# Performance work log

Hardware: AMD Instinct MI355X
Metric: run time of the kernel (lower is better)

The kernel has to match this reference:

```python
import jax, jax.numpy as jnp
import numpy as np

B, S, D = 2, 2048, 2048
H, KVH, DH = 32, 8, 64
G = H // KVH  # num_key_value_groups
SCALE = DH ** -0.5
NEG = -1e9


def rotate_half(x):
    x1, x2 = jnp.split(x, 2, axis=-1)
    return jnp.concatenate([-x2, x1], axis=-1)


def setup_inputs() -> dict:
    key = jax.random.key(0)
    ks = jax.random.split(key, 6)
    hidden_states = jax.random.normal(ks[0], (B, S, D), dtype=jnp.float32)
    # RoPE tables (base 10000), shape [B, S, DH]
    inv_freq = 1.0 / (10000.0 ** (np.arange(0, DH, 2, dtype=np.float32) / DH))
    t = np.arange(S, dtype=np.float32)
    freqs = np.outer(t, inv_freq)                     # [S, DH/2]
    emb = np.concatenate([freqs, freqs], axis=-1)     # [S, DH]
    cos = jnp.broadcast_to(jnp.cos(emb)[None], (B, S, DH)).astype(jnp.float32)
    sin = jnp.broadcast_to(jnp.sin(emb)[None], (B, S, DH)).astype(jnp.float32)
    # additive causal mask [B, 1, S, S]
    causal = np.tril(np.ones((S, S), dtype=bool))
    mask = jnp.asarray(np.where(causal, 0.0, NEG).astype(np.float32))
    attention_mask = jnp.broadcast_to(mask[None, None], (B, 1, S, S))
    std = 0.02
    Wq = jax.random.normal(ks[1], (H * DH, D), dtype=jnp.float32) * std
    Wk = jax.random.normal(ks[2], (KVH * DH, D), dtype=jnp.float32) * std
    Wv = jax.random.normal(ks[3], (KVH * DH, D), dtype=jnp.float32) * std
    Wo = jax.random.normal(ks[4], (D, H * DH), dtype=jnp.float32) * std
    return {"hidden_states": hidden_states, "cos": cos, "sin": sin,
            "attention_mask": attention_mask, "Wq": Wq, "Wk": Wk, "Wv": Wv, "Wo": Wo}


def reference(hidden_states, cos, sin, attention_mask, Wq, Wk, Wv, Wo):
    b, s, d = hidden_states.shape
    # projections -> [B, heads, S, DH]
    q = (hidden_states @ Wq.T).reshape(b, s, H, DH).transpose(0, 2, 1, 3)
    k = (hidden_states @ Wk.T).reshape(b, s, KVH, DH).transpose(0, 2, 1, 3)
    v = (hidden_states @ Wv.T).reshape(b, s, KVH, DH).transpose(0, 2, 1, 3)
    # RoPE (unsqueeze_dim=1)
    c = cos[:, None]  # [B,1,S,DH]
    sn = sin[:, None]
    q = q * c + rotate_half(q) * sn
    k = k * c + rotate_half(k) * sn
    # GQA: repeat kv heads
    k = jnp.repeat(k, G, axis=1)
    v = jnp.repeat(v, G, axis=1)
    scores = jnp.einsum("bhqd,bhkd->bhqk", q, k) * SCALE + attention_mask
    attn = jax.nn.softmax(scores.astype(jnp.float32), axis=-1).astype(q.dtype)
    out = jnp.einsum("bhqk,bhkd->bhqd", attn, v)          # [B,H,S,DH]
    out = out.transpose(0, 2, 1, 3).reshape(b, s, H * DH)  # [B,S,H*DH]
    return out @ Wo.T
```

## Files before the change

kernel.cpp:

```cpp
#include <hip/hip_runtime.h>

typedef unsigned short u16;
typedef __attribute__((ext_vector_type(8))) short s16x8;
typedef __attribute__((ext_vector_type(4))) float f32x4;
typedef __attribute__((ext_vector_type(4))) unsigned short u16x4;

#define MFMA16(a, b, c) __builtin_amdgcn_mfma_f32_16x16x32_bf16(a, b, c, 0, 0, 0)

__device__ __forceinline__ u16 f2bf(float f) {
  unsigned u = __builtin_bit_cast(unsigned, f);
  u += 0x7fffu + ((u >> 16) & 1u);
  return (u16)(u >> 16);
}

__device__ __forceinline__ u16 f2bf_fast(float f) {
  return (u16)((__builtin_bit_cast(unsigned, f) + 0x8000u) >> 16);
}

__device__ __forceinline__ void async16(const void* g, void* l) {
  __builtin_amdgcn_global_load_lds(
      (const __attribute__((address_space(1))) void*)g,
      (__attribute__((address_space(3))) void*)l, 16, 0, 0);
}

__device__ __forceinline__ s16x8 ld8(const u16* p) { return *(const s16x8*)p; }

#define PRE 0.18033688011112042f

__global__ __launch_bounds__(256) void cvt_all(
    const float* __restrict__ X, const float* __restrict__ Wq,
    const float* __restrict__ Wk, const float* __restrict__ Wv,
    const float* __restrict__ Wo, u16* __restrict__ out) {
  long e = (long)(blockIdx.x * 256 + threadIdx.x) * 4;
  const float* src;
  if (e < 8388608L) src = X + e;
  else if (e < 12582912L) src = Wq + (e - 8388608L);
  else if (e < 13631488L) src = Wk + (e - 12582912L);
  else if (e < 14680064L) src = Wv + (e - 13631488L);
  else src = Wo + (e - 14680064L);
  float4 v = *(const float4*)src;
  u16x4 o = {f2bf(v.x), f2bf(v.y), f2bf(v.z), f2bf(v.w)};
  *(u16x4*)(out + e) = o;
}

enum { EPI_QKV = 0, EPI_OUT = 1 };

template <int EPI>
__global__ __launch_bounds__(256) void gemm_nt(
    const u16* __restrict__ A, const u16* __restrict__ Bm,
    const float* __restrict__ cosp, const float* __restrict__ sinp,
    u16* __restrict__ Qo, u16* __restrict__ Ko, u16* __restrict__ Vo,
    float* __restrict__ Co, int K) {
  __shared__ u16 SM[16384];
  const int t = threadIdx.x;
  const int lane = t & 63;
  const int w = t >> 6, wm = w >> 1, wn = w & 1;
  const int quad = lane >> 4, c16 = lane & 15;
  const int m0 = blockIdx.y * 128, n0 = blockIdx.x * 128;

  f32x4 acc[4][4];
  const f32x4 zero = {0.f, 0.f, 0.f, 0.f};
#pragma unroll
  for (int i = 0; i < 4; ++i)
#pragma unroll
    for (int j = 0; j < 4; ++j) acc[i][j] = zero;

  const u16* gA[2];
  const u16* gB[2];
  int lof[2];
#pragma unroll
  for (int p = 0; p < 2; ++p) {
    int c = t + p * 256;
    int dr = c >> 3, k8 = (c & 7) ^ (dr & 7);
    int row = 2 * dr + (k8 >> 2), col = (k8 & 3) * 8;
    gA[p] = A + (size_t)(m0 + row) * K + col;
    gB[p] = Bm + (size_t)(n0 + row) * K + col;
    lof[p] = c * 8;
  }

  int aoff[4], boff[4];
#pragma unroll
  for (int i = 0; i < 4; ++i) {
    int rowA = wm * 64 + i * 16 + c16;
    int drA = rowA >> 1;
    int chA = (((rowA & 1) << 2) | quad) ^ (drA & 7);
    aoff[i] = drA * 64 + chA * 8;
    int rowB = wn * 64 + i * 16 + c16;
    int drB = rowB >> 1;
    int chB = (((rowB & 1) << 2) | quad) ^ (drB & 7);
    boff[i] = 4096 + drB * 64 + chB * 8;
  }

#pragma unroll
  for (int p = 0; p < 2; ++p) {
    async16(gA[p], &SM[lof[p]]);
    async16(gB[p], &SM[4096 + lof[p]]);
  }

  const int niter = K >> 5;
  for (int kt = 0; kt < niter; ++kt) {
    const int cb = (kt & 1) * 8192;
    __syncthreads();
    if (kt + 1 < niter) {
      const int nb = 8192 - cb;
#pragma unroll
      for (int p = 0; p < 2; ++p) {
        gA[p] += 32;
        gB[p] += 32;
        async16(gA[p], &SM[nb + lof[p]]);
        async16(gB[p], &SM[nb + 4096 + lof[p]]);
      }
    }
    s16x8 af[4], bfr[4];
#pragma unroll
    for (int i = 0; i < 4; ++i) af[i] = ld8(&SM[cb + aoff[i]]);
#pragma unroll
    for (int j = 0; j < 4; ++j) bfr[j] = ld8(&SM[cb + boff[j]]);
#pragma unroll
    for (int i = 0; i < 4; ++i)
#pragma unroll
      for (int j = 0; j < 4; ++j) acc[i][j] = MFMA16(af[i], bfr[j], acc[i][j]);
  }

  if (EPI == EPI_OUT) {
#pragma unroll
    for (int i = 0; i < 4; ++i)
#pragma unroll
      for (int r = 0; r < 4; ++r) {
        int m = m0 + wm * 64 + i * 16 + quad * 4 + r;
        float* dst = Co + (size_t)m * 2048 + n0 + wn * 64 + c16;
#pragma unroll
        for (int j = 0; j < 4; ++j) dst[j * 16] = acc[i][j][r];
      }
  } else if (n0 >= 2560) {
    __syncthreads();
#pragma unroll
    for (int i = 0; i < 4; ++i)
#pragma unroll
      for (int r = 0; r < 4; ++r) {
        int sl = wm * 64 + i * 16 + quad * 4 + r;
#pragma unroll
        for (int j = 0; j < 4; ++j) {
          int dl = wn * 64 + j * 16 + c16;
          SM[dl * 128 + (((sl >> 3) ^ (dl & 15)) * 8) + (sl & 7)] =
              f2bf(acc[i][j][r]);
        }
      }
    __syncthreads();
    int bb = m0 >> 11, m0s = m0 & 2047;
#pragma unroll
    for (int p = 0; p < 8; ++p) {
      int q = p * 256 + t;
      int dl = q >> 4, k = q & 15;
      s16x8 vrow = ld8(&SM[dl * 128 + ((k ^ (dl & 15)) * 8)]);
      int nab = n0 + dl;
      int kvh = (nab - 2560) >> 6, dh = nab & 63;
      *(s16x8*)(Vo + ((size_t)(bb * 8 + kvh) * 64 + dh) * 2048 + m0s + k * 8) =
          vrow;
    }
  } else {
    const int nbase = n0 + wn * 64;
#pragma unroll
    for (int i = 0; i < 4; ++i)
#pragma unroll
      for (int r = 0; r < 4; ++r) {
        int m = m0 + wm * 64 + i * 16 + quad * 4 + r;
        int b = m >> 11, s = m & 2047;
        if (nbase < 2048) {
          int h = nbase >> 6;
          size_t base = ((size_t)(b * 32 + h) * 2048 + s) * 64;
#pragma unroll
          for (int j = 0; j < 2; ++j) {
            int d = j * 16 + c16;
            float v1 = acc[i][j][r], v2 = acc[i][j + 2][r];
            float c1 = cosp[m * 64 + d], s1 = sinp[m * 64 + d];
            float c2 = cosp[m * 64 + d + 32], s2 = sinp[m * 64 + d + 32];
            Qo[base + d] = f2bf((v1 * c1 - v2 * s1) * PRE);
            Qo[base + d + 32] = f2bf((v2 * c2 + v1 * s2) * PRE);
          }
        } else {
          int h = (nbase - 2048) >> 6;
          size_t base = ((size_t)(b * 8 + h) * 2048 + s) * 64;
#pragma unroll
          for (int j = 0; j < 2; ++j) {
            int d = j * 16 + c16;
            float v1 = acc[i][j][r], v2 = acc[i][j + 2][r];
            float c1 = cosp[m * 64 + d], s1 = sinp[m * 64 + d];
            float c2 = cosp[m * 64 + d + 32], s2 = sinp[m * 64 + d + 32];
            Ko[base + d] = f2bf(v1 * c1 - v2 * s1);
            Ko[base + d + 32] = f2bf(v2 * c2 + v1 * s2);
          }
        }
      }
  }
}

__global__ __launch_bounds__(256) void attn(const u16* __restrict__ Q,
                                            const u16* __restrict__ Kg,
                                            const u16* __restrict__ Vg,
                                            u16* __restrict__ O) {
  __shared__ u16 Ks[2][4096];
  __shared__ u16 Vs[2][4096];
  __shared__ u16 Ps[8192];
  const int t = threadIdx.x;
  const int lane = t & 63;
  const int w = t >> 6;
  const int quad = lane >> 4, c16 = lane & 15;
  const int bh = blockIdx.y;
  const int b = bh >> 5, h = bh & 31;
  const int kvh = h >> 2;

  const u16* Qbase = Q + ((size_t)(b * 32 + h) * 2048) * 64;
  const u16* Kbase = Kg + ((size_t)(b * 8 + kvh) * 2048) * 64;
  const u16* Vbase = Vg + ((size_t)(b * 8 + kvh) * 64) * 2048;

  const int sr0 = t >> 3, sc0 = ((t & 7) ^ (sr0 & 7)) * 8;
  const int sr1 = (t + 256) >> 3, sc1 = (((t + 256) & 7) ^ (sr1 & 7)) * 8;

  for (int ph = 0; ph < 2; ++ph) {
    const int qt = ph ? 15 - blockIdx.x : blockIdx.x;
    const int q0 = qt * 128;

    s16x8 qa[2][2];
#pragma unroll
    for (int im = 0; im < 2; ++im)
#pragma unroll
      for (int c = 0; c < 2; ++c)
        qa[im][c] = ld8(Qbase + (size_t)(q0 + w * 32 + im * 16 + c16) * 64 +
                        c * 32 + quad * 8);

    f32x4 oacc[2][4];
    const f32x4 zero = {0.f, 0.f, 0.f, 0.f};
    float lacc[2][4];
#pragma unroll
    for (int im = 0; im < 2; ++im)
#pragma unroll
      for (int r = 0; r < 4; ++r) lacc[im][r] = 0.f;
#pragma unroll
    for (int im = 0; im < 2; ++im)
#pragma unroll
      for (int dt = 0; dt < 4; ++dt) oacc[im][dt] = zero;

    const int nkt = 2 * qt + 2;

    __syncthreads();
    {
      const u16* kg = Kbase;
      async16(kg + sr0 * 64 + sc0, &Ks[0][t * 8]);
      async16(kg + sr1 * 64 + sc1, &Ks[0][t * 8 + 2048]);
      async16(Vbase + (size_t)sr0 * 2048 + sc0, &Vs[0][t * 8]);
      async16(Vbase + (size_t)sr1 * 2048 + sc1, &Vs[0][t * 8 + 2048]);
    }

    for (int kt = 0; kt < nkt; ++kt) {
      const int cur = kt & 1;
      __syncthreads();
      if (kt + 1 < nkt) {
        const int nxt = 1 - cur;
        const u16* kg = Kbase + (kt + 1) * 4096;
        async16(kg + sr0 * 64 + sc0, &Ks[nxt][t * 8]);
        async16(kg + sr1 * 64 + sc1, &Ks[nxt][t * 8 + 2048]);
        async16(Vbase + (size_t)sr0 * 2048 + (kt + 1) * 64 + sc0,
                &Vs[nxt][t * 8]);
        async16(Vbase + (size_t)sr1 * 2048 + (kt + 1) * 64 + sc1,
                &Vs[nxt][t * 8 + 2048]);
      }
      const u16* Kb = Ks[cur];
      const u16* Vb = Vs[cur];

#pragma unroll
      for (int im = 0; im < 2; ++im) {
        f32x4 sc[4];
#pragma unroll
        for (int in = 0; in < 4; ++in) sc[in] = zero;
#pragma unroll
        for (int c = 0; c < 2; ++c)
#pragma unroll
          for (int in = 0; in < 4; ++in) {
            s16x8 kf = ld8(&Kb[(in * 16 + c16) * 64 +
                               (((c * 4 + quad) ^ (c16 & 7)) * 8)]);
            sc[in] = MFMA16(qa[im][c], kf, sc[in]);
          }
        const int rbase = q0 + w * 32 + im * 16;
        if (kt * 64 + 63 > rbase) {
#pragma unroll
          for (int in = 0; in < 4; ++in) {
            int kcol = kt * 64 + in * 16 + c16;
#pragma unroll
            for (int r = 0; r < 4; ++r)
              if (kcol > rbase + quad * 4 + r) sc[in][r] = -1e30f;
          }
        }
#pragma unroll
        for (int in = 0; in < 4; ++in)
#pragma unroll
          for (int r = 0; r < 4; ++r) {
            float p = exp2f(sc[in][r]);
            lacc[im][r] += p;
            int row = im * 16 + quad * 4 + r;
            Ps[w * 2048 + row * 64 +
               (((in * 2 + (c16 >> 3)) ^ (row & 7)) * 8) + (c16 & 7)] =
                f2bf_fast(p);
          }
      }

#pragma unroll
      for (int c = 0; c < 2; ++c) {
        const int swz = ((c * 4 + quad) ^ (c16 & 7)) * 8;
        s16x8 pf[2];
#pragma unroll
        for (int im = 0; im < 2; ++im)
          pf[im] = ld8(&Ps[w * 2048 + (im * 16 + c16) * 64 + swz]);
#pragma unroll
        for (int dt = 0; dt < 4; ++dt) {
          s16x8 vf = ld8(&Vb[(dt * 16 + c16) * 64 + swz]);
#pragma unroll
          for (int im = 0; im < 2; ++im)
            oacc[im][dt] = MFMA16(pf[im], vf, oacc[im][dt]);
        }
      }
    }

#pragma unroll
    for (int im = 0; im < 2; ++im) {
      float inv[4];
#pragma unroll
      for (int r = 0; r < 4; ++r) {
        float v = lacc[im][r];
        v += __shfl_xor(v, 1);
        v += __shfl_xor(v, 2);
        v += __shfl_xor(v, 4);
        v += __shfl_xor(v, 8);
        inv[r] = 1.f / v;
      }
#pragma unroll
      for (int dt = 0; dt < 4; ++dt)
#pragma unroll
        for (int r = 0; r < 4; ++r) {
          int s = q0 + w * 32 + im * 16 + quad * 4 + r;
          O[((size_t)(b * 2048 + s)) * 2048 + h * 64 + dt * 16 + c16] =
              f2bf(oacc[im][dt][r] * inv[r]);
        }
    }
  }
}

extern "C" void kernel_launch(void* const* d_in, const int* in_sizes, int n_in,
                              void* d_out, int out_size, void* d_ws,
                              size_t ws_size, hipStream_t stream) {
  const float* X = (const float*)d_in[0];
  const float* cosp = (const float*)d_in[1];
  const float* sinp = (const float*)d_in[2];
  const float* Wq = (const float*)d_in[4];
  const float* Wk = (const float*)d_in[5];
  const float* Wv = (const float*)d_in[6];
  const float* Wo = (const float*)d_in[7];
  float* out = (float*)d_out;

  u16* Xb = (u16*)d_ws;
  u16* Wqkv = Xb + 8388608;
  u16* Wob = Wqkv + 6291456;
  u16* Qr = Wob + 4194304;
  u16* Kr = Qr + 8388608;
  u16* Vt = Kr + 2097152;
  u16* Ob = Vt + 2097152;

  cvt_all<<<18432, 256, 0, stream>>>(X, Wq, Wk, Wv, Wo, Xb);

  gemm_nt<EPI_QKV><<<dim3(24, 32), 256, 0, stream>>>(
      Xb, Wqkv, cosp, sinp, Qr, Kr, Vt, nullptr, 2048);

  attn<<<dim3(8, 64), 256, 0, stream>>>(Qr, Kr, Vt, Ob);

  gemm_nt<EPI_OUT><<<dim3(16, 32), 256, 0, stream>>>(
      Ob, Wob, nullptr, nullptr, nullptr, nullptr, nullptr, out, 2048);
}
```

Before: 328.5 us.

## Rewrite attention inner loop with 32x32 MFMA and register-resident P via permlane swap

The attention kernel switches from 16x16x32 to 32x32x16 bf16 MFMAs and computes S transposed (K times Q), so each lane holds scores for a single query row. Probabilities are packed to bf16 with v_cvt_pk_bf16_f32 and rearranged across half-waves with permlane32_swap to form the PV operand directly in registers, removing the P round trip through shared memory. Fully masked 32-key sub-blocks are skipped and the row-sum reduction becomes one shuffle plus a small LDS broadcast. The risks are higher register pressure from the 16-wide accumulators and a fragile lane and register mapping.

```diff
diff --git a/kernel.cpp b/kernel.cpp
--- a/kernel.cpp
+++ b/kernel.cpp
@@ -3,9 +3,12 @@
 typedef unsigned short u16;
 typedef __attribute__((ext_vector_type(8))) short s16x8;
 typedef __attribute__((ext_vector_type(4))) float f32x4;
+typedef __attribute__((ext_vector_type(16))) float f32x16;
 typedef __attribute__((ext_vector_type(4))) unsigned short u16x4;
+typedef __attribute__((ext_vector_type(4))) unsigned int u32x4;
 
 #define MFMA16(a, b, c) __builtin_amdgcn_mfma_f32_16x16x32_bf16(a, b, c, 0, 0, 0)
+#define MFMA32(a, b, c) __builtin_amdgcn_mfma_f32_32x32x16_bf16(a, b, c, 0, 0, 0)
 
 __device__ __forceinline__ u16 f2bf(float f) {
   unsigned u = __builtin_bit_cast(unsigned, f);
@@ -13,10 +16,6 @@
   return (u16)(u >> 16);
 }
 
-__device__ __forceinline__ u16 f2bf_fast(float f) {
-  return (u16)((__builtin_bit_cast(unsigned, f) + 0x8000u) >> 16);
-}
-
 __device__ __forceinline__ void async16(const void* g, void* l) {
   __builtin_amdgcn_global_load_lds(
       (const __attribute__((address_space(1))) void*)g,
@@ -24,6 +23,12 @@
 }
 
 __device__ __forceinline__ s16x8 ld8(const u16* p) { return *(const s16x8*)p; }
+
+__device__ __forceinline__ unsigned cvtpk(float lo, float hi) {
+  unsigned r;
+  asm("v_cvt_pk_bf16_f32 %0, %1, %2" : "=v"(r) : "v"(lo), "v"(hi));
+  return r;
+}
 
 #define PRE 0.18033688011112042f
 
@@ -201,11 +206,11 @@
                                             u16* __restrict__ O) {
   __shared__ u16 Ks[2][4096];
   __shared__ u16 Vs[2][4096];
-  __shared__ u16 Ps[8192];
+  __shared__ float Lred[128];
   const int t = threadIdx.x;
   const int lane = t & 63;
   const int w = t >> 6;
-  const int quad = lane >> 4, c16 = lane & 15;
+  const int l31 = lane & 31, hi = lane >> 5;
   const int bh = blockIdx.y;
   const int b = bh >> 5, h = bh & 31;
   const int kvh = h >> 2;
@@ -217,37 +222,35 @@
   const int sr0 = t >> 3, sc0 = ((t & 7) ^ (sr0 & 7)) * 8;
   const int sr1 = (t + 256) >> 3, sc1 = (((t + 256) & 7) ^ (sr1 & 7)) * 8;
 
+  int off8[4];
+#pragma unroll
+  for (int c = 0; c < 4; ++c) off8[c] = ((2 * c + hi) ^ (l31 & 7)) * 8;
+  const int rbB = l31 * 64;
+
   for (int ph = 0; ph < 2; ++ph) {
     const int qt = ph ? 15 - blockIdx.x : blockIdx.x;
     const int q0 = qt * 128;
-
-    s16x8 qa[2][2];
-#pragma unroll
-    for (int im = 0; im < 2; ++im)
-#pragma unroll
-      for (int c = 0; c < 2; ++c)
-        qa[im][c] = ld8(Qbase + (size_t)(q0 + w * 32 + im * 16 + c16) * 64 +
-                        c * 32 + quad * 8);
-
-    f32x4 oacc[2][4];
-    const f32x4 zero = {0.f, 0.f, 0.f, 0.f};
-    float lacc[2][4];
-#pragma unroll
-    for (int im = 0; im < 2; ++im)
-#pragma unroll
-      for (int r = 0; r < 4; ++r) lacc[im][r] = 0.f;
-#pragma unroll
-    for (int im = 0; im < 2; ++im)
-#pragma unroll
-      for (int dt = 0; dt < 4; ++dt) oacc[im][dt] = zero;
+    const int rbase = q0 + w * 32;
+    const int qrow = rbase + l31;
+
+    s16x8 qf[4];
+#pragma unroll
+    for (int dc = 0; dc < 4; ++dc)
+      qf[dc] = ld8(Qbase + (size_t)qrow * 64 + dc * 16 + hi * 8);
+
+    f32x16 oacc[2];
+#pragma unroll
+    for (int dn = 0; dn < 2; ++dn)
+#pragma unroll
+      for (int r = 0; r < 16; ++r) oacc[dn][r] = 0.f;
+    float lacc = 0.f;
 
     const int nkt = 2 * qt + 2;
 
     __syncthreads();
     {
-      const u16* kg = Kbase;
-      async16(kg + sr0 * 64 + sc0, &Ks[0][t * 8]);
-      async16(kg + sr1 * 64 + sc1, &Ks[0][t * 8 + 2048]);
+      async16(Kbase + sr0 * 64 + sc0, &Ks[0][t * 8]);
+      async16(Kbase + sr1 * 64 + sc1, &Ks[0][t * 8 + 2048]);
       async16(Vbase + (size_t)sr0 * 2048 + sc0, &Vs[0][t * 8]);
       async16(Vbase + (size_t)sr1 * 2048 + sc1, &Vs[0][t * 8 + 2048]);
     }
@@ -269,78 +272,71 @@
       const u16* Vb = Vs[cur];
 
 #pragma unroll
-      for (int im = 0; im < 2; ++im) {
-        f32x4 sc[4];
-#pragma unroll
-        for (int in = 0; in < 4; ++in) sc[in] = zero;
-#pragma unroll
-        for (int c = 0; c < 2; ++c)
-#pragma unroll
-          for (int in = 0; in < 4; ++in) {
-            s16x8 kf = ld8(&Kb[(in * 16 + c16) * 64 +
-                               (((c * 4 + quad) ^ (c16 & 7)) * 8)]);
-            sc[in] = MFMA16(qa[im][c], kf, sc[in]);
-          }
-        const int rbase = q0 + w * 32 + im * 16;
-        if (kt * 64 + 63 > rbase) {
-#pragma unroll
-          for (int in = 0; in < 4; ++in) {
-            int kcol = kt * 64 + in * 16 + c16;
-#pragma unroll
-            for (int r = 0; r < 4; ++r)
-              if (kcol > rbase + quad * 4 + r) sc[in][r] = -1e30f;
+      for (int kn = 0; kn < 2; ++kn) {
+        const int kb0 = kt * 64 + kn * 32;
+        if (kb0 <= rbase + 31) {
+          f32x16 s_;
+#pragma unroll
+          for (int r = 0; r < 16; ++r) s_[r] = 0.f;
+#pragma unroll
+          for (int dc = 0; dc < 4; ++dc) {
+            s16x8 kf = ld8(&Kb[kn * 2048 + rbB + off8[dc]]);
+            s_ = MFMA32(kf, qf[dc], s_);
+          }
+          if (kb0 + 31 > rbase) {
+            const int kb = kb0 + 4 * hi;
+#pragma unroll
+            for (int r = 0; r < 16; ++r)
+              if (kb + (r & 3) + 8 * (r >> 2) > qrow) s_[r] = -1e30f;
+          }
+          float p[16];
+#pragma unroll
+          for (int r = 0; r < 16; ++r) p[r] = __builtin_amdgcn_exp2f(s_[r]);
+          {
+            float e0 = p[0] + p[1], e1 = p[2] + p[3], e2 = p[4] + p[5],
+                  e3 = p[6] + p[7], e4 = p[8] + p[9], e5 = p[10] + p[11],
+                  e6 = p[12] + p[13], e7 = p[14] + p[15];
+            lacc += ((e0 + e1) + (e2 + e3)) + ((e4 + e5) + (e6 + e7));
+          }
+#pragma unroll
+          for (int c2 = 0; c2 < 2; ++c2) {
+            unsigned a0 = cvtpk(p[8 * c2 + 0], p[8 * c2 + 1]);
+            unsigned b0 = cvtpk(p[8 * c2 + 4], p[8 * c2 + 5]);
+            unsigned a1 = cvtpk(p[8 * c2 + 2], p[8 * c2 + 3]);
+            unsigned b1 = cvtpk(p[8 * c2 + 6], p[8 * c2 + 7]);
+            auto s0 = __builtin_amdgcn_permlane32_swap(a0, b0, false, false);
+            auto s1 = __builtin_amdgcn_permlane32_swap(a1, b1, false, false);
+            u32x4 fw = {(unsigned)s0[0], (unsigned)s1[0], (unsigned)s0[1],
+                        (unsigned)s1[1]};
+            s16x8 F = __builtin_bit_cast(s16x8, fw);
+            const int kk = 2 * kn + c2;
+#pragma unroll
+            for (int dn = 0; dn < 2; ++dn) {
+              s16x8 vf = ld8(&Vb[dn * 2048 + rbB + off8[kk]]);
+              oacc[dn] = MFMA32(F, vf, oacc[dn]);
+            }
           }
         }
-#pragma unroll
-        for (int in = 0; in < 4; ++in)
-#pragma unroll
-          for (int r = 0; r < 4; ++r) {
-            float p = exp2f(sc[in][r]);
-            lacc[im][r] += p;
-            int row = im * 16 + quad * 4 + r;
-            Ps[w * 2048 + row * 64 +
-               (((in * 2 + (c16 >> 3)) ^ (row & 7)) * 8) + (c16 & 7)] =
-                f2bf_fast(p);
-          }
-      }
-
-#pragma unroll
-      for (int c = 0; c < 2; ++c) {
-        const int swz = ((c * 4 + quad) ^ (c16 & 7)) * 8;
-        s16x8 pf[2];
-#pragma unroll
-        for (int im = 0; im < 2; ++im)
-          pf[im] = ld8(&Ps[w * 2048 + (im * 16 + c16) * 64 + swz]);
-#pragma unroll
-        for (int dt = 0; dt < 4; ++dt) {
-          s16x8 vf = ld8(&Vb[(dt * 16 + c16) * 64 + swz]);
-#pragma unroll
-          for (int im = 0; im < 2; ++im)
-            oacc[im][dt] = MFMA16(pf[im], vf, oacc[im][dt]);
-        }
-      }
-    }
-
-#pragma unroll
-    for (int im = 0; im < 2; ++im) {
-      float inv[4];
-#pragma unroll
-      for (int r = 0; r < 4; ++r) {
-        float v = lacc[im][r];
-        v += __shfl_xor(v, 1);
-        v += __shfl_xor(v, 2);
-        v += __shfl_xor(v, 4);
-        v += __shfl_xor(v, 8);
-        inv[r] = 1.f / v;
-      }
-#pragma unroll
-      for (int dt = 0; dt < 4; ++dt)
-#pragma unroll
-        for (int r = 0; r < 4; ++r) {
-          int s = q0 + w * 32 + im * 16 + quad * 4 + r;
-          O[((size_t)(b * 2048 + s)) * 2048 + h * 64 + dt * 16 + c16] =
-              f2bf(oacc[im][dt][r] * inv[r]);
-        }
+      }
+    }
+
+    {
+      float ltot = lacc + __shfl_xor(lacc, 32);
+      if (lane < 32) Lred[w * 32 + l31] = 1.f / ltot;
+      f32x4 lv[4];
+#pragma unroll
+      for (int g = 0; g < 4; ++g)
+        lv[g] = *(const f32x4*)&Lred[w * 32 + 8 * g + 4 * hi];
+#pragma unroll
+      for (int dn = 0; dn < 2; ++dn)
+#pragma unroll
+        for (int g = 0; g < 4; ++g)
+#pragma unroll
+          for (int j = 0; j < 4; ++j) {
+            int s = rbase + 8 * g + 4 * hi + j;
+            O[((size_t)(b * 2048 + s)) * 2048 + h * 64 + dn * 32 + l31] =
+                f2bf(oacc[dn][4 * g + j] * lv[g][j]);
+          }
     }
   }
 }
```

After: 314.6 us. -4.2%, faster.
